# Optimization experiments

Measured on AMD Instinct MI355X. Metric: run time of the kernel, lower is better.

The kernel has to match this reference:

```python
import jax, jax.numpy as jnp
import numpy as np

N_NODES = 50000
N_EDGES = 800000
IN_CH = 64
HID = 128
OUT = 1


def setup_inputs() -> dict:
    key = jax.random.key(0)
    ks = jax.random.split(key, 8)
    x = jax.random.normal(ks[0], (N_NODES, IN_CH), dtype=jnp.float32)
    edge_index = jax.random.randint(ks[1], (2, N_EDGES), 0, N_NODES, dtype=jnp.int64)
    def lin(k, fan_in, fan_out):
        s = 1.0 / np.sqrt(fan_in)
        return jax.random.uniform(k, (fan_in, fan_out), jnp.float32, -s, s)
    W1 = lin(ks[2], IN_CH, HID)
    W2 = lin(ks[3], HID, HID)
    W3 = lin(ks[4], HID, HID)
    W4 = lin(ks[5], HID, HID)
    Wout = lin(ks[6], HID, OUT)
    z = lambda n: jnp.zeros((n,), jnp.float32)
    return {"x": x, "edge_index": edge_index,
            "W1": W1, "b1": z(HID), "W2": W2, "b2": z(HID),
            "W3": W3, "b3": z(HID), "W4": W4, "b4": z(HID),
            "Wout": Wout, "bout": z(OUT)}


def _gin_conv(x, src, dst, Wa, ba, Wb, bb):
    # GINConv with eps=0: h_i = MLP(x_i + sum_{j->i} x_j)
    msgs = jnp.take(x, src, axis=0)                      # [E, d] gather
    agg = jax.ops.segment_sum(msgs, dst, num_segments=x.shape[0])  # [N, d]
    h = x + agg
    h = jnp.maximum(h @ Wa + ba, 0.0) @ Wb + bb
    return h


def reference(x, edge_index, W1, b1, W2, b2, W3, b3, W4, b4, Wout, bout):
    src, dst = edge_index[0], edge_index[1]
    h = _gin_conv(x, src, dst, W1, b1, W2, b2)
    h = jnp.maximum(h, 0.0)
    h = _gin_conv(h, src, dst, W3, b3, W4, b4)
    h = jnp.maximum(h, 0.0)
    return h @ Wout + bout
```

## Files before the change

kernel.cpp:

```cpp
#include <hip/hip_runtime.h>


#define N_NODES 50000
#define IN_CH 64
#define HID 128
#define REGION 6250

typedef short short8 __attribute__((ext_vector_type(8)));
typedef float f32x4 __attribute__((ext_vector_type(4)));

__device__ __forceinline__ unsigned bf16_rne(float f) {
    unsigned u = __float_as_uint(f);
    return (u + 0x7FFFu + ((u >> 16) & 1u)) >> 16;
}
__device__ __forceinline__ float lo_f(unsigned u) { return __uint_as_float(u << 16); }
__device__ __forceinline__ float hi_f(unsigned u) { return __uint_as_float(u & 0xFFFF0000u); }

__global__ void detect64_kernel(const int* __restrict__ ei32, int* __restrict__ flag) {
    int t = threadIdx.x;
    int v = ei32[2 * t + 1];
    unsigned long long b = __ballot(v != 0);
    __shared__ unsigned long long r[4];
    if ((t & 63) == 0) r[t >> 6] = b;
    __syncthreads();
    if (t == 0) flag[0] = ((r[0] | r[1] | r[2] | r[3]) == 0ULL) ? 1 : 0;
}

__device__ __forceinline__ int load_idx(const void* ei, int is64, int pos) {
    if (is64) return (int)((const long long*)ei)[pos];
    return ((const int*)ei)[pos];
}

__global__ __launch_bounds__(256) void compact_kernel(
    const void* __restrict__ ei, const int* __restrict__ is64,
    ushort* __restrict__ srcs, ushort* __restrict__ dsts, int E)
{
    int i64 = *is64;
    for (int e = blockIdx.x * 256 + threadIdx.x; e < E; e += gridDim.x * 256) {
        srcs[e] = (ushort)load_idx(ei, i64, e);
        dsts[e] = (ushort)load_idx(ei, i64, E + e);
    }
}

__global__ __launch_bounds__(256) void hist8_kernel(
    const ushort* __restrict__ dsts, int* __restrict__ deg, int E, int nsub)
{
    int g   = blockIdx.x & 7;
    int sub = blockIdx.x >> 3;
    int lo = g * REGION, hi = lo + REGION;
    for (int e = sub * 256 + threadIdx.x; e < E; e += nsub * 256) {
        int d = dsts[e];
        if (d >= lo && d < hi) atomicAdd(&deg[d], 1);
    }
}

__global__ __launch_bounds__(256) void fill8_kernel(
    const ushort* __restrict__ srcs, const ushort* __restrict__ dsts,
    int* __restrict__ cursor, ushort* __restrict__ col, int E, int nsub)
{
    int g   = blockIdx.x & 7;
    int sub = blockIdx.x >> 3;
    int lo = g * REGION, hi = lo + REGION;
    for (int e = sub * 256 + threadIdx.x; e < E; e += nsub * 256) {
        int d = dsts[e];
        if (d >= lo && d < hi) {
            int pos = atomicAdd(&cursor[d], 1);
            col[pos] = srcs[e];
        }
    }
}

__device__ __forceinline__ int wave_incl_scan(int v, int lane) {
    #pragma unroll
    for (int off = 1; off < 64; off <<= 1) {
        int u = __shfl_up(v, off);
        if (lane >= off) v += u;
    }
    return v;
}

__global__ __launch_bounds__(256) void scan1_kernel(
    const int* __restrict__ deg, int* __restrict__ incl,
    int* __restrict__ bsum, int N)
{
    int i = blockIdx.x * 256 + threadIdx.x;
    int lane = threadIdx.x & 63;
    int w = threadIdx.x >> 6;
    int v = (i < N) ? deg[i] : 0;
    int s = wave_incl_scan(v, lane);
    __shared__ int wsum[4];
    if (lane == 63) wsum[w] = s;
    __syncthreads();
    int off = 0;
    #pragma unroll
    for (int k = 0; k < 4; k++) if (k < w) off += wsum[k];
    s += off;
    if (i < N) incl[i] = s;
    if (threadIdx.x == 255) bsum[blockIdx.x] = s;
}

__global__ __launch_bounds__(256) void scan2_kernel(
    const int* __restrict__ bsum, int* __restrict__ bsx, int nb)
{
    int t = threadIdx.x;
    int lane = t & 63;
    int w = t >> 6;
    int v = (t < nb) ? bsum[t] : 0;
    int s = wave_incl_scan(v, lane);
    __shared__ int wsum[4];
    if (lane == 63) wsum[w] = s;
    __syncthreads();
    int off = 0;
    #pragma unroll
    for (int k = 0; k < 4; k++) if (k < w) off += wsum[k];
    s += off;
    if (t < nb) bsx[t] = s - v;
}

__global__ __launch_bounds__(256) void scan3_kernel(
    int* __restrict__ deg_cursor, int* __restrict__ incl_rowptr,
    const int* __restrict__ bsx, int N)
{
    int i = blockIdx.x * 256 + threadIdx.x;
    if (i >= N) return;
    int incl = incl_rowptr[i] + bsx[blockIdx.x];
    int d = deg_cursor[i];
    int excl = incl - d;
    incl_rowptr[i] = excl;
    deg_cursor[i] = excl;
    if (i == N - 1) incl_rowptr[N] = incl;
}

__global__ __launch_bounds__(256) void xconv_kernel(
    const float* __restrict__ x, ushort* __restrict__ xb, int total4)
{
    int i = blockIdx.x * 256 + threadIdx.x;
    if (i >= total4) return;
    float4 v = ((const float4*)x)[i];
    ushort4 o;
    o.x = (ushort)bf16_rne(v.x); o.y = (ushort)bf16_rne(v.y);
    o.z = (ushort)bf16_rne(v.z); o.w = (ushort)bf16_rne(v.w);
    ((ushort4*)xb)[i] = o;
}

__global__ __launch_bounds__(256) void wconv_all_kernel(
    const float* __restrict__ W1, const float* __restrict__ W2,
    const float* __restrict__ W3, const float* __restrict__ W4,
    ushort* __restrict__ w1t, ushort* __restrict__ w2t,
    ushort* __restrict__ w3t, ushort* __restrict__ w4t)
{
    int i = blockIdx.x * 256 + threadIdx.x;
    if (i < 8192) {
        int n = i >> 6, k = i & 63;
        w1t[i] = (ushort)bf16_rne(W1[(size_t)k * 128 + n]);
    } else if (i < 8192 + 16384) {
        int j = i - 8192; int n = j >> 7, k = j & 127;
        w2t[j] = (ushort)bf16_rne(W2[(size_t)k * 128 + n]);
    } else if (i < 8192 + 32768) {
        int j = i - 8192 - 16384; int n = j >> 7, k = j & 127;
        w3t[j] = (ushort)bf16_rne(W3[(size_t)k * 128 + n]);
    } else if (i < 8192 + 49152) {
        int j = i - 8192 - 32768; int n = j >> 7, k = j & 127;
        w4t[j] = (ushort)bf16_rne(W4[(size_t)k * 128 + n]);
    }
}

__global__ __launch_bounds__(256) void gather64_kernel(
    const ushort* __restrict__ xb, const int* __restrict__ rp,
    const ushort* __restrict__ col, ushort* __restrict__ outb, int N)
{
    const unsigned* xu = (const unsigned*)xb;
    unsigned* outu = (unsigned*)outb;
    int wid = (blockIdx.x * blockDim.x + threadIdx.x) >> 6;
    int lane = threadIdx.x & 63;
    int half = lane >> 5, cl = lane & 31;
    if (wid >= N) return;
    int b = rp[wid], e2 = rp[wid + 1];
    unsigned us = xu[(size_t)wid * 32 + cl];
    float ax = (half == 0) ? lo_f(us) : 0.f;
    float ay = (half == 0) ? hi_f(us) : 0.f;
    for (int base = b; base < e2; base += 64) {
        int cnt = e2 - base; if (cnt > 64) cnt = 64;
        int myc = (base + lane < e2) ? (int)col[base + lane] : 0;
        for (int j = 0; j < cnt; j += 2) {
            int jj = j + half;
            int s = __shfl(myc, jj);
            unsigned u = xu[(size_t)s * 32 + cl];
            if (jj < cnt) { ax += lo_f(u); ay += hi_f(u); }
        }
    }
    ax += __shfl_xor(ax, 32);
    ay += __shfl_xor(ay, 32);
    if (half == 0) outu[(size_t)wid * 32 + cl] = bf16_rne(ax) | (bf16_rne(ay) << 16);
}

__global__ __launch_bounds__(256) void gather128_kernel(
    const ushort* __restrict__ in, const int* __restrict__ rp,
    const ushort* __restrict__ col, ushort* __restrict__ outb, int N)
{
    const unsigned* inu = (const unsigned*)in;
    unsigned* outu = (unsigned*)outb;
    int wid = (blockIdx.x * blockDim.x + threadIdx.x) >> 6;
    int lane = threadIdx.x & 63;
    if (wid >= N) return;
    int b = rp[wid], e2 = rp[wid + 1];
    unsigned u0 = inu[(size_t)wid * 64 + lane];
    float ax = lo_f(u0), ay = hi_f(u0);
    float bx = 0.f, by = 0.f;
    for (int base = b; base < e2; base += 64) {
        int cnt = e2 - base; if (cnt > 64) cnt = 64;
        int myc = (base + lane < e2) ? (int)col[base + lane] : 0;
        int j = 0;
        for (; j + 3 < cnt; j += 4) {
            int s0 = __shfl(myc, j),     s1 = __shfl(myc, j + 1);
            int s2 = __shfl(myc, j + 2), s3 = __shfl(myc, j + 3);
            unsigned ua = inu[(size_t)s0 * 64 + lane];
            unsigned ub = inu[(size_t)s1 * 64 + lane];
            unsigned uc = inu[(size_t)s2 * 64 + lane];
            unsigned ud = inu[(size_t)s3 * 64 + lane];
            ax += lo_f(ua); ay += hi_f(ua);
            bx += lo_f(ub); by += hi_f(ub);
            ax += lo_f(uc); ay += hi_f(uc);
            bx += lo_f(ud); by += hi_f(ud);
        }
        for (; j < cnt; j++) {
            int s = __shfl(myc, j);
            unsigned u = inu[(size_t)s * 64 + lane];
            ax += lo_f(u); ay += hi_f(u);
        }
    }
    ax += bx; ay += by;
    outu[(size_t)wid * 64 + lane] = bf16_rne(ax) | (bf16_rne(ay) << 16);
}

template<int K1, bool HEAD>
__global__ __launch_bounds__(256) void mlp_fused_kernel(
    const ushort* __restrict__ A, const ushort* __restrict__ W1t,
    const ushort* __restrict__ W2t, const float* __restrict__ b1,
    const float* __restrict__ b2, ushort* __restrict__ outb,
    const float* __restrict__ Wout, const float* __restrict__ bout,
    float* __restrict__ fout, int N)
{
    constexpr int SA = K1 + 8;
    __shared__ __align__(16) ushort Asm[64 * SA];
    __shared__ __align__(16) ushort Wsm[128 * 136];
    __shared__ __align__(16) ushort T1s[64 * 136];

    const int t  = threadIdx.x;
    const int n0 = blockIdx.x * 64;
    const int w  = t >> 6, l = t & 63;
    const int lr = l & 15, lg = l >> 4;

    {
        int row = t >> 2, seg = t & 3;
        int n = n0 + row; int nc = n < N ? n : N - 1;
        const uint4* src = (const uint4*)(A + (size_t)nc * K1 + seg * (K1 / 4));
        uint4* dst = (uint4*)&Asm[row * SA + seg * (K1 / 4)];
        #pragma unroll
        for (int q = 0; q < K1 / 32; q++) dst[q] = src[q];
    }
    {
        int n = t >> 1, half = t & 1;
        const uint4* src = (const uint4*)(W1t + (size_t)n * K1 + half * (K1 / 2));
        uint4* dst = (uint4*)&Wsm[n * SA + half * (K1 / 2)];
        #pragma unroll
        for (int q = 0; q < K1 / 16; q++) dst[q] = src[q];
    }
    __syncthreads();

    f32x4 acc[8];
    #pragma unroll
    for (int c = 0; c < 8; c++) acc[c] = (f32x4){0.f, 0.f, 0.f, 0.f};
    #pragma unroll
    for (int ks = 0; ks < K1 / 32; ks++) {
        short8 a = *(const short8*)&Asm[(w * 16 + lr) * SA + ks * 32 + lg * 8];
        #pragma unroll
        for (int c = 0; c < 8; c++) {
            short8 bb = *(const short8*)&Wsm[(c * 16 + lr) * SA + ks * 32 + lg * 8];
            acc[c] = __builtin_amdgcn_mfma_f32_16x16x32_bf16(a, bb, acc[c], 0, 0, 0);
        }
    }
    #pragma unroll
    for (int c = 0; c < 8; c++) {
        float bc = b1[c * 16 + lr];
        #pragma unroll
        for (int j = 0; j < 4; j++) {
            float v = fmaxf(acc[c][j] + bc, 0.f);
            T1s[(w * 16 + lg * 4 + j) * 136 + c * 16 + lr] = (ushort)bf16_rne(v);
        }
    }
    __syncthreads();

    {
        int n = t >> 1, half = t & 1;
        const uint4* src = (const uint4*)(W2t + (size_t)n * 128 + half * 64);
        uint4* dst = (uint4*)&Wsm[n * 136 + half * 64];
        #pragma unroll
        for (int q = 0; q < 8; q++) dst[q] = src[q];
    }
    __syncthreads();

    #pragma unroll
    for (int c = 0; c < 8; c++) acc[c] = (f32x4){0.f, 0.f, 0.f, 0.f};
    #pragma unroll
    for (int ks = 0; ks < 4; ks++) {
        short8 a = *(const short8*)&T1s[(w * 16 + lr) * 136 + ks * 32 + lg * 8];
        #pragma unroll
        for (int c = 0; c < 8; c++) {
            short8 bb = *(const short8*)&Wsm[(c * 16 + lr) * 136 + ks * 32 + lg * 8];
            acc[c] = __builtin_amdgcn_mfma_f32_16x16x32_bf16(a, bb, acc[c], 0, 0, 0);
        }
    }
    if (HEAD) {
        float wv[8];
        #pragma unroll
        for (int c = 0; c < 8; c++) wv[c] = Wout[c * 16 + lr];
        float p[4] = {0.f, 0.f, 0.f, 0.f};
        #pragma unroll
        for (int c = 0; c < 8; c++) {
            float bc = b2[c * 16 + lr];
            #pragma unroll
            for (int j = 0; j < 4; j++) {
                float v = fmaxf(acc[c][j] + bc, 0.f);
                p[j] += v * wv[c];
            }
        }
        #pragma unroll
        for (int j = 0; j < 4; j++)
            #pragma unroll
            for (int off = 1; off < 16; off <<= 1) p[j] += __shfl_xor(p[j], off);
        if (lr == 0) {
            int row0 = n0 + w * 16 + lg * 4;
            float bo = bout[0];
            #pragma unroll
            for (int j = 0; j < 4; j++)
                if (row0 + j < N) fout[row0 + j] = p[j] + bo;
        }
    } else {
        #pragma unroll
        for (int c = 0; c < 8; c++) {
            float bc = b2[c * 16 + lr];
            #pragma unroll
            for (int j = 0; j < 4; j++) {
                int row = n0 + w * 16 + lg * 4 + j;
                if (row < N) {
                    float v = fmaxf(acc[c][j] + bc, 0.f);
                    outb[(size_t)row * 128 + c * 16 + lr] = (ushort)bf16_rne(v);
                }
            }
        }
    }
}

extern "C" void kernel_launch(void* const* d_in, const int* in_sizes, int n_in,
                              void* d_out, int out_size, void* d_ws, size_t ws_size,
                              hipStream_t stream) {
    const float* x    = (const float*)d_in[0];
    const void*  ei   = d_in[1];
    const float* W1   = (const float*)d_in[2];
    const float* b1   = (const float*)d_in[3];
    const float* W2   = (const float*)d_in[4];
    const float* b2   = (const float*)d_in[5];
    const float* W3   = (const float*)d_in[6];
    const float* b3   = (const float*)d_in[7];
    const float* W4   = (const float*)d_in[8];
    const float* b4   = (const float*)d_in[9];
    const float* Wout = (const float*)d_in[10];
    const float* bout = (const float*)d_in[11];
    float* out = (float*)d_out;

    const int E = in_sizes[1] / 2;
    const int N = N_NODES;
    const int nb = (N + 255) / 256;

    char* wsb = (char*)d_ws;
    size_t off = 0;
    auto alloc = [&](size_t bytes) -> void* {
        void* p = wsb + off;
        off = (off + bytes + 255) & ~(size_t)255;
        return p;
    };
    int*    flag   = (int*)alloc(4);
    int*    deg    = (int*)alloc((size_t)N * 4);
    int*    rowptr = (int*)alloc((size_t)(N + 1) * 4);
    int*    bsum   = (int*)alloc(256 * 4);
    int*    bsx    = (int*)alloc(256 * 4);
    ushort* srcs16 = (ushort*)alloc((size_t)E * 2);
    ushort* dsts16 = (ushort*)alloc((size_t)E * 2);
    ushort* col    = (ushort*)alloc((size_t)E * 2);
    ushort* xb     = (ushort*)alloc((size_t)N * 64 * 2);
    ushort* w1t    = (ushort*)alloc(128 * 64 * 2);
    ushort* w2t    = (ushort*)alloc(128 * 128 * 2);
    ushort* w3t    = (ushort*)alloc(128 * 128 * 2);
    ushort* w4t    = (ushort*)alloc(128 * 128 * 2);
    ushort* agg1   = (ushort*)alloc((size_t)N * 64 * 2);
    ushort* h1     = (ushort*)alloc((size_t)N * 128 * 2);
    ushort* agg2   = (ushort*)alloc((size_t)N * 128 * 2);

    detect64_kernel<<<1, 256, 0, stream>>>((const int*)ei, flag);

    hipMemsetAsync(deg, 0, (size_t)N * sizeof(int), stream);
    compact_kernel<<<1024, 256, 0, stream>>>(ei, flag, srcs16, dsts16, E);
    hist8_kernel<<<2048, 256, 0, stream>>>(dsts16, deg, E, 256);
    scan1_kernel<<<nb, 256, 0, stream>>>(deg, rowptr, bsum, N);
    scan2_kernel<<<1, 256, 0, stream>>>(bsum, bsx, nb);
    scan3_kernel<<<nb, 256, 0, stream>>>(deg, rowptr, bsx, N);
    fill8_kernel<<<2048, 256, 0, stream>>>(srcs16, dsts16, deg, col, E, 256);

    xconv_kernel<<<(N * 64 / 4 + 255) / 256, 256, 0, stream>>>(x, xb, N * 64 / 4);
    wconv_all_kernel<<<(8192 + 49152 + 255) / 256, 256, 0, stream>>>(
        W1, W2, W3, W4, w1t, w2t, w3t, w4t);

    const int agg_blocks = (N * 64 + 255) / 256;
    const int mlp_blocks = (N + 63) / 64;

    gather64_kernel<<<agg_blocks, 256, 0, stream>>>(xb, rowptr, col, agg1, N);
    mlp_fused_kernel<64, false><<<mlp_blocks, 256, 0, stream>>>(
        agg1, w1t, w2t, b1, b2, h1, nullptr, nullptr, nullptr, N);

    gather128_kernel<<<agg_blocks, 256, 0, stream>>>(h1, rowptr, col, agg2, N);
    mlp_fused_kernel<128, true><<<mlp_blocks, 256, 0, stream>>>(
        agg2, w3t, w4t, b3, b4, nullptr, Wout, bout, out, N);
}
```

Baseline: 274.8 us.

## Merge setup kernels, deepen gather unrolling, and alias MLP shared memory

Folds the int64 detection and the degree memset into the compact kernel, and merges the two-level block scan into a single kernel where each block reduces its preceding block sums. It also merges the x and weight bf16 conversions into one launch. The gather kernels are unrolled to eight outstanding neighbor loads per iteration, and the fused MLP reuses one shared buffer for the A tile and the intermediate T1 tile, with a barrier moved accordingly. The aim is fewer launches, more memory-level parallelism and less LDS per block, at the cost of redundant per-block detection and prefix work plus higher register pressure.

```diff
diff --git a/kernel.cpp b/kernel.cpp
--- a/kernel.cpp
+++ b/kernel.cpp
@@ -16,29 +16,27 @@
 __device__ __forceinline__ float lo_f(unsigned u) { return __uint_as_float(u << 16); }
 __device__ __forceinline__ float hi_f(unsigned u) { return __uint_as_float(u & 0xFFFF0000u); }
 
-__global__ void detect64_kernel(const int* __restrict__ ei32, int* __restrict__ flag) {
+__global__ __launch_bounds__(256) void compact_kernel(
+    const int* __restrict__ ei32, ushort* __restrict__ srcs,
+    ushort* __restrict__ dsts, int* __restrict__ deg, int E, int N)
+{
     int t = threadIdx.x;
     int v = ei32[2 * t + 1];
     unsigned long long b = __ballot(v != 0);
     __shared__ unsigned long long r[4];
     if ((t & 63) == 0) r[t >> 6] = b;
     __syncthreads();
-    if (t == 0) flag[0] = ((r[0] | r[1] | r[2] | r[3]) == 0ULL) ? 1 : 0;
-}
-
-__device__ __forceinline__ int load_idx(const void* ei, int is64, int pos) {
-    if (is64) return (int)((const long long*)ei)[pos];
-    return ((const int*)ei)[pos];
-}
-
-__global__ __launch_bounds__(256) void compact_kernel(
-    const void* __restrict__ ei, const int* __restrict__ is64,
-    ushort* __restrict__ srcs, ushort* __restrict__ dsts, int E)
-{
-    int i64 = *is64;
-    for (int e = blockIdx.x * 256 + threadIdx.x; e < E; e += gridDim.x * 256) {
-        srcs[e] = (ushort)load_idx(ei, i64, e);
-        dsts[e] = (ushort)load_idx(ei, i64, E + e);
+    int is64 = ((r[0] | r[1] | r[2] | r[3]) == 0ULL) ? 1 : 0;
+
+    for (int i = blockIdx.x * 256 + t; i < N; i += gridDim.x * 256) deg[i] = 0;
+
+    const long long* p64 = (const long long*)ei32;
+    for (int e = blockIdx.x * 256 + t; e < E; e += gridDim.x * 256) {
+        int s, d;
+        if (is64) { s = (int)p64[e]; d = (int)p64[E + e]; }
+        else      { s = ei32[e];     d = ei32[E + e]; }
+        srcs[e] = (ushort)s;
+        dsts[e] = (ushort)d;
     }
 }
 
@@ -99,31 +97,24 @@
     if (threadIdx.x == 255) bsum[blockIdx.x] = s;
 }
 
-__global__ __launch_bounds__(256) void scan2_kernel(
-    const int* __restrict__ bsum, int* __restrict__ bsx, int nb)
+__global__ __launch_bounds__(256) void scan3b_kernel(
+    int* __restrict__ deg_cursor, int* __restrict__ incl_rowptr,
+    const int* __restrict__ bsum, int N, int nb)
 {
     int t = threadIdx.x;
     int lane = t & 63;
     int w = t >> 6;
-    int v = (t < nb) ? bsum[t] : 0;
-    int s = wave_incl_scan(v, lane);
-    __shared__ int wsum[4];
-    if (lane == 63) wsum[w] = s;
-    __syncthreads();
-    int off = 0;
-    #pragma unroll
-    for (int k = 0; k < 4; k++) if (k < w) off += wsum[k];
-    s += off;
-    if (t < nb) bsx[t] = s - v;
-}
-
-__global__ __launch_bounds__(256) void scan3_kernel(
-    int* __restrict__ deg_cursor, int* __restrict__ incl_rowptr,
-    const int* __restrict__ bsx, int N)
-{
-    int i = blockIdx.x * 256 + threadIdx.x;
+    int v = (t < nb && t < blockIdx.x) ? bsum[t] : 0;
+    #pragma unroll
+    for (int off = 32; off; off >>= 1) v += __shfl_down(v, off);
+    __shared__ int ws[4];
+    if (lane == 0) ws[w] = v;
+    __syncthreads();
+    int pref = ws[0] + ws[1] + ws[2] + ws[3];
+
+    int i = blockIdx.x * 256 + t;
     if (i >= N) return;
-    int incl = incl_rowptr[i] + bsx[blockIdx.x];
+    int incl = incl_rowptr[i] + pref;
     int d = deg_cursor[i];
     int excl = incl - d;
     incl_rowptr[i] = excl;
@@ -131,37 +122,37 @@
     if (i == N - 1) incl_rowptr[N] = incl;
 }
 
-__global__ __launch_bounds__(256) void xconv_kernel(
-    const float* __restrict__ x, ushort* __restrict__ xb, int total4)
-{
-    int i = blockIdx.x * 256 + threadIdx.x;
-    if (i >= total4) return;
-    float4 v = ((const float4*)x)[i];
-    ushort4 o;
-    o.x = (ushort)bf16_rne(v.x); o.y = (ushort)bf16_rne(v.y);
-    o.z = (ushort)bf16_rne(v.z); o.w = (ushort)bf16_rne(v.w);
-    ((ushort4*)xb)[i] = o;
-}
-
-__global__ __launch_bounds__(256) void wconv_all_kernel(
+#define XITEMS (N_NODES * IN_CH / 4)
+__global__ __launch_bounds__(256) void conv_all_kernel(
+    const float* __restrict__ x,
     const float* __restrict__ W1, const float* __restrict__ W2,
     const float* __restrict__ W3, const float* __restrict__ W4,
+    ushort* __restrict__ xb,
     ushort* __restrict__ w1t, ushort* __restrict__ w2t,
     ushort* __restrict__ w3t, ushort* __restrict__ w4t)
 {
     int i = blockIdx.x * 256 + threadIdx.x;
-    if (i < 8192) {
-        int n = i >> 6, k = i & 63;
-        w1t[i] = (ushort)bf16_rne(W1[(size_t)k * 128 + n]);
-    } else if (i < 8192 + 16384) {
-        int j = i - 8192; int n = j >> 7, k = j & 127;
-        w2t[j] = (ushort)bf16_rne(W2[(size_t)k * 128 + n]);
-    } else if (i < 8192 + 32768) {
-        int j = i - 8192 - 16384; int n = j >> 7, k = j & 127;
-        w3t[j] = (ushort)bf16_rne(W3[(size_t)k * 128 + n]);
-    } else if (i < 8192 + 49152) {
-        int j = i - 8192 - 32768; int n = j >> 7, k = j & 127;
-        w4t[j] = (ushort)bf16_rne(W4[(size_t)k * 128 + n]);
+    if (i < XITEMS) {
+        float4 v = ((const float4*)x)[i];
+        ushort4 o;
+        o.x = (ushort)bf16_rne(v.x); o.y = (ushort)bf16_rne(v.y);
+        o.z = (ushort)bf16_rne(v.z); o.w = (ushort)bf16_rne(v.w);
+        ((ushort4*)xb)[i] = o;
+        return;
+    }
+    int j = i - XITEMS;
+    if (j < 8192) {
+        int n = j >> 6, k = j & 63;
+        w1t[j] = (ushort)bf16_rne(W1[(size_t)k * 128 + n]);
+    } else if (j < 8192 + 16384) {
+        int q = j - 8192; int n = q >> 7, k = q & 127;
+        w2t[q] = (ushort)bf16_rne(W2[(size_t)k * 128 + n]);
+    } else if (j < 8192 + 32768) {
+        int q = j - 8192 - 16384; int n = q >> 7, k = q & 127;
+        w3t[q] = (ushort)bf16_rne(W3[(size_t)k * 128 + n]);
+    } else if (j < 8192 + 49152) {
+        int q = j - 8192 - 32768; int n = q >> 7, k = q & 127;
+        w4t[q] = (ushort)bf16_rne(W4[(size_t)k * 128 + n]);
     }
 }
 
@@ -182,7 +173,22 @@
     for (int base = b; base < e2; base += 64) {
         int cnt = e2 - base; if (cnt > 64) cnt = 64;
         int myc = (base + lane < e2) ? (int)col[base + lane] : 0;
-        for (int j = 0; j < cnt; j += 2) {
+        int j = 0;
+        for (; j + 7 < cnt; j += 8) {
+            int s0 = __shfl(myc, j +     half);
+            int s1 = __shfl(myc, j + 2 + half);
+            int s2 = __shfl(myc, j + 4 + half);
+            int s3 = __shfl(myc, j + 6 + half);
+            unsigned u0 = xu[(size_t)s0 * 32 + cl];
+            unsigned u1 = xu[(size_t)s1 * 32 + cl];
+            unsigned u2 = xu[(size_t)s2 * 32 + cl];
+            unsigned u3 = xu[(size_t)s3 * 32 + cl];
+            ax += lo_f(u0); ay += hi_f(u0);
+            ax += lo_f(u1); ay += hi_f(u1);
+            ax += lo_f(u2); ay += hi_f(u2);
+            ax += lo_f(u3); ay += hi_f(u3);
+        }
+        for (; j < cnt; j += 2) {
             int jj = j + half;
             int s = __shfl(myc, jj);
             unsigned u = xu[(size_t)s * 32 + cl];
@@ -211,17 +217,27 @@
         int cnt = e2 - base; if (cnt > 64) cnt = 64;
         int myc = (base + lane < e2) ? (int)col[base + lane] : 0;
         int j = 0;
-        for (; j + 3 < cnt; j += 4) {
+        for (; j + 7 < cnt; j += 8) {
             int s0 = __shfl(myc, j),     s1 = __shfl(myc, j + 1);
             int s2 = __shfl(myc, j + 2), s3 = __shfl(myc, j + 3);
-            unsigned ua = inu[(size_t)s0 * 64 + lane];
-            unsigned ub = inu[(size_t)s1 * 64 + lane];
-            unsigned uc = inu[(size_t)s2 * 64 + lane];
-            unsigned ud = inu[(size_t)s3 * 64 + lane];
-            ax += lo_f(ua); ay += hi_f(ua);
-            bx += lo_f(ub); by += hi_f(ub);
-            ax += lo_f(uc); ay += hi_f(uc);
-            bx += lo_f(ud); by += hi_f(ud);
+            int s4 = __shfl(myc, j + 4), s5 = __shfl(myc, j + 5);
+            int s6 = __shfl(myc, j + 6), s7 = __shfl(myc, j + 7);
+            unsigned va = inu[(size_t)s0 * 64 + lane];
+            unsigned vb = inu[(size_t)s1 * 64 + lane];
+            unsigned vc = inu[(size_t)s2 * 64 + lane];
+            unsigned vd = inu[(size_t)s3 * 64 + lane];
+            unsigned ve = inu[(size_t)s4 * 64 + lane];
+            unsigned vf = inu[(size_t)s5 * 64 + lane];
+            unsigned vg = inu[(size_t)s6 * 64 + lane];
+            unsigned vh = inu[(size_t)s7 * 64 + lane];
+            ax += lo_f(va); ay += hi_f(va);
+            bx += lo_f(vb); by += hi_f(vb);
+            ax += lo_f(vc); ay += hi_f(vc);
+            bx += lo_f(vd); by += hi_f(vd);
+            ax += lo_f(ve); ay += hi_f(ve);
+            bx += lo_f(vf); by += hi_f(vf);
+            ax += lo_f(vg); ay += hi_f(vg);
+            bx += lo_f(vh); by += hi_f(vh);
         }
         for (; j < cnt; j++) {
             int s = __shfl(myc, j);
@@ -242,9 +258,10 @@
     float* __restrict__ fout, int N)
 {
     constexpr int SA = K1 + 8;
-    __shared__ __align__(16) ushort Asm[64 * SA];
-    __shared__ __align__(16) ushort Wsm[128 * 136];
-    __shared__ __align__(16) ushort T1s[64 * 136];
+    __shared__ __align__(16) ushort lds[(64 + 128) * 136];
+    ushort* Asm = lds;
+    ushort* T1s = lds;
+    ushort* Wsm = lds + 64 * 136;
 
     const int t  = threadIdx.x;
     const int n0 = blockIdx.x * 64;
@@ -280,6 +297,8 @@
             acc[c] = __builtin_amdgcn_mfma_f32_16x16x32_bf16(a, bb, acc[c], 0, 0, 0);
         }
     }
+    __syncthreads();
+
     #pragma unroll
     for (int c = 0; c < 8; c++) {
         float bc = b1[c * 16 + lr];
@@ -289,8 +308,6 @@
             T1s[(w * 16 + lg * 4 + j) * 136 + c * 16 + lr] = (ushort)bf16_rne(v);
         }
     }
-    __syncthreads();
-
     {
         int n = t >> 1, half = t & 1;
         const uint4* src = (const uint4*)(W2t + (size_t)n * 128 + half * 64);
@@ -356,7 +373,7 @@
                               void* d_out, int out_size, void* d_ws, size_t ws_size,
                               hipStream_t stream) {
     const float* x    = (const float*)d_in[0];
-    const void*  ei   = d_in[1];
+    const int*   ei   = (const int*)d_in[1];
     const float* W1   = (const float*)d_in[2];
     const float* b1   = (const float*)d_in[3];
     const float* W2   = (const float*)d_in[4];
@@ -380,11 +397,9 @@
         off = (off + bytes + 255) & ~(size_t)255;
         return p;
     };
-    int*    flag   = (int*)alloc(4);
     int*    deg    = (int*)alloc((size_t)N * 4);
     int*    rowptr = (int*)alloc((size_t)(N + 1) * 4);
     int*    bsum   = (int*)alloc(256 * 4);
-    int*    bsx    = (int*)alloc(256 * 4);
     ushort* srcs16 = (ushort*)alloc((size_t)E * 2);
     ushort* dsts16 = (ushort*)alloc((size_t)E * 2);
     ushort* col    = (ushort*)alloc((size_t)E * 2);
@@ -397,19 +412,14 @@
     ushort* h1     = (ushort*)alloc((size_t)N * 128 * 2);
     ushort* agg2   = (ushort*)alloc((size_t)N * 128 * 2);
 
-    detect64_kernel<<<1, 256, 0, stream>>>((const int*)ei, flag);
-
-    hipMemsetAsync(deg, 0, (size_t)N * sizeof(int), stream);
-    compact_kernel<<<1024, 256, 0, stream>>>(ei, flag, srcs16, dsts16, E);
+    compact_kernel<<<1024, 256, 0, stream>>>(ei, srcs16, dsts16, deg, E, N);
     hist8_kernel<<<2048, 256, 0, stream>>>(dsts16, deg, E, 256);
     scan1_kernel<<<nb, 256, 0, stream>>>(deg, rowptr, bsum, N);
-    scan2_kernel<<<1, 256, 0, stream>>>(bsum, bsx, nb);
-    scan3_kernel<<<nb, 256, 0, stream>>>(deg, rowptr, bsx, N);
+    scan3b_kernel<<<nb, 256, 0, stream>>>(deg, rowptr, bsum, N, nb);
     fill8_kernel<<<2048, 256, 0, stream>>>(srcs16, dsts16, deg, col, E, 256);
 
-    xconv_kernel<<<(N * 64 / 4 + 255) / 256, 256, 0, stream>>>(x, xb, N * 64 / 4);
-    wconv_all_kernel<<<(8192 + 49152 + 255) / 256, 256, 0, stream>>>(
-        W1, W2, W3, W4, w1t, w2t, w3t, w4t);
+    conv_all_kernel<<<(XITEMS + 57344 + 255) / 256, 256, 0, stream>>>(
+        x, W1, W2, W3, W4, xb, w1t, w2t, w3t, w4t);
 
     const int agg_blocks = (N * 64 + 255) / 256;
     const int mlp_blocks = (N + 63) / 64;
```

After: 249.4 us. 1.1x faster.
